# Kernel optimization log

Hardware: AMD Instinct MI355X
Metric: run time of the kernel (lower is better)

Reference implementation:

```python
import jax, jax.numpy as jnp
import numpy as np

N_USERS = 100000
N_ITEMS = 50000
N = N_USERS + N_ITEMS
D = 64
NNZ = 2000000
N_HOPS = 3
EDGE_RATE = 0.5   # note: torch code KEEPS an edge with prob = rate (floor(rate+u))
MESS_RATE = 0.1   # standard dropout: keep prob = 1 - rate


def setup_inputs() -> dict:
    key = jax.random.key(0)
    k1, k2, k3, k4, k5 = jax.random.split(key, 5)
    user_embed = jax.random.normal(k1, (N_USERS, D), dtype=jnp.float32) * 0.1
    item_embed = jax.random.normal(k2, (N_ITEMS, D), dtype=jnp.float32) * 0.1
    edge_rows = jax.random.randint(k3, (NNZ,), 0, N, dtype=jnp.int32)
    edge_cols = jax.random.randint(k4, (NNZ,), 0, N, dtype=jnp.int32)
    edge_vals = jax.random.uniform(k5, (NNZ,), dtype=jnp.float32)
    return {"user_embed": user_embed, "item_embed": item_embed,
            "edge_vals": edge_vals, "edge_rows": edge_rows, "edge_cols": edge_cols}


def reference(user_embed, item_embed, edge_vals, edge_rows, edge_cols):
    # all_embed: [N, D]
    all_embed = jnp.concatenate([user_embed, item_embed], axis=0)
    agg = all_embed
    embs = [all_embed]
    dkey = jax.random.key(42)
    for hop in range(N_HOPS):
        dkey, ke, km = jax.random.split(dkey, 3)
        # sparse edge dropout: torch keeps edge where floor(rate + u) == 1, i.e. u >= 1 - rate
        u = jax.random.uniform(ke, (NNZ,), dtype=jnp.float32)
        keep = (EDGE_RATE + u) >= 1.0
        v = jnp.where(keep, edge_vals, 0.0) * (1.0 / (1.0 - EDGE_RATE))
        # spmm: out[r] += v * agg[c]   -- gather + segment-reduce
        msg = v[:, None] * agg[edge_cols]          # [NNZ, D]
        agg = jax.ops.segment_sum(msg, edge_rows, num_segments=N)  # [N, D]
        # message dropout (standard inverted dropout, p = MESS_RATE)
        mk = jax.random.bernoulli(km, 1.0 - MESS_RATE, agg.shape)
        agg = jnp.where(mk, agg * (1.0 / (1.0 - MESS_RATE)), 0.0)
        embs.append(agg)
    # [N, n_hops+1, D]; user half = out[:N_USERS], item half = out[N_USERS:]
    return jnp.stack(embs, axis=1)
```

## Files before the change

### kernel.cpp

```cpp
#include <hip/hip_runtime.h>
#include <stdint.h>

#define N_USERS 100000
#define N_ITEMS 50000
#define NTOT    150000
#define DIM     64
#define NNZ     2000000
#define NHOPS   3
#define NBLK_SCAN ((NTOT + 255) / 256)
#define NOCT    8
#define OCT_ROWS (NTOT / NOCT)
#define NBUCK   293
#define BCAP    6400
#define HB_ITERS 8

__host__ __device__ inline void tf2x32(uint32_t k0, uint32_t k1,
                                       uint32_t x0, uint32_t x1,
                                       uint32_t& o0, uint32_t& o1) {
  uint32_t ks2 = k0 ^ k1 ^ 0x1BD11BDAu;
  x0 += k0; x1 += k1;
#define ROTL(x,r) (((x) << (r)) | ((x) >> (32 - (r))))
#define RND(r) { x0 += x1; x1 = ROTL(x1, r); x1 ^= x0; }
  RND(13) RND(15) RND(26) RND(6)
  x0 += k1;  x1 += ks2 + 1u;
  RND(17) RND(29) RND(16) RND(24)
  x0 += ks2; x1 += k0 + 2u;
  RND(13) RND(15) RND(26) RND(6)
  x0 += k0;  x1 += k1 + 3u;
  RND(17) RND(29) RND(16) RND(24)
  x0 += k1;  x1 += ks2 + 4u;
  RND(13) RND(15) RND(26) RND(6)
  x0 += ks2; x1 += k0 + 5u;
  o0 = x0; o1 = x1;
#undef RND
#undef ROTL
}

__device__ inline float tf_uniform(uint32_t k0, uint32_t k1, uint32_t idx) {
  uint32_t b1, b2;
  tf2x32(k0, k1, 0u, idx, b1, b2);
  uint32_t bits = b1 ^ b2;
  return __uint_as_float((bits >> 9) | 0x3f800000u) - 1.0f;
}

__device__ inline uint32_t keep_bits(uint32_t e,
                                     uint32_t e00, uint32_t e01,
                                     uint32_t e10, uint32_t e11,
                                     uint32_t e20, uint32_t e21) {
  uint32_t kb = 0u;
  if (0.5f + tf_uniform(e00, e01, e) >= 1.0f) kb |= 1u;
  if (0.5f + tf_uniform(e10, e11, e) >= 1.0f) kb |= 2u;
  if (0.5f + tf_uniform(e20, e21, e) >= 1.0f) kb |= 4u;
  return kb;
}


__global__ __launch_bounds__(256) void k_init(const float4* __restrict__ user,
                                              const float4* __restrict__ item,
                                              float4* __restrict__ out) {
  int idx = blockIdx.x * 256 + threadIdx.x;
  if (idx >= NTOT * 16) return;
  int n = idx >> 4;
  float4 v = (n < N_USERS) ? user[idx] : item[idx - N_USERS * 16];
  out[(size_t)n * 64 + (idx & 15)] = v;
}

__global__ __launch_bounds__(256) void k_hist_bin(const int* __restrict__ rows,
                                                  const int* __restrict__ cols,
                                                  const float* __restrict__ vals,
                                                  uint32_t* __restrict__ cnt,
                                                  uint32_t* __restrict__ gbcur,
                                                  uint2* __restrict__ staging,
                                                  uint32_t e00, uint32_t e01,
                                                  uint32_t e10, uint32_t e11,
                                                  uint32_t e20, uint32_t e21) {
  __shared__ uint32_t bcnt[NBUCK], bbase[NBUCK];
  int t = threadIdx.x;
  int ebase = blockIdx.x * (HB_ITERS * 256);
  for (int b = t; b < NBUCK; b += 256) bcnt[b] = 0u;
  __syncthreads();

  uint32_t srow[HB_ITERS], scol[HB_ITERS], sval[HB_ITERS];
#pragma unroll
  for (int it = 0; it < HB_ITERS; ++it) {
    int e = ebase + it * 256 + t;
    bool valid = (e < NNZ);
    uint32_t kb = valid ? keep_bits((uint32_t)e, e00, e01, e10, e11, e20, e21) : 0u;
    uint32_t row = 0, colkb = 0, v2b = 0;
    if (kb) {
      row = (uint32_t)rows[e];
      colkb = ((uint32_t)cols[e] << 3) | kb;
      v2b = __float_as_uint(vals[e] * 2.0f);
      atomicAdd(&cnt[row], 1u);
      atomicAdd(&bcnt[row >> 9], 1u);
    }
    srow[it] = row; scol[it] = colkb; sval[it] = v2b;
  }
  __syncthreads();
  for (int b = t; b < NBUCK; b += 256) {
    uint32_t c = bcnt[b];
    bbase[b] = c ? atomicAdd(&gbcur[b * 16], c) : 0u;
    bcnt[b] = 0u;
  }
  __syncthreads();
#pragma unroll
  for (int it = 0; it < HB_ITERS; ++it) {
    uint32_t colkb = scol[it];
    if (colkb & 7u) {
      uint32_t row = srow[it];
      uint32_t b = row >> 9;
      uint32_t rank = atomicAdd(&bcnt[b], 1u);
      staging[(size_t)b * BCAP + bbase[b] + rank] =
          make_uint2(((row & 511u) << 21) | colkb, sval[it]);
    }
  }
}

__global__ __launch_bounds__(256) void k_scan1(const uint32_t* __restrict__ cnt,
                                               uint32_t* __restrict__ strt,
                                               uint32_t* __restrict__ part) {
  __shared__ uint32_t s[256];
  int t = threadIdx.x;
  int i = blockIdx.x * 256 + t;
  uint32_t x = (i < NTOT) ? cnt[i] : 0u;
  s[t] = x; __syncthreads();
  for (int off = 1; off < 256; off <<= 1) {
    uint32_t y = (t >= off) ? s[t - off] : 0u;
    __syncthreads();
    s[t] += y;
    __syncthreads();
  }
  if (i < NTOT) strt[i] = s[t] - x;
  if (t == 255) part[blockIdx.x] = s[255];
}

__global__ __launch_bounds__(1024) void k_scan2(uint32_t* __restrict__ part) {
  __shared__ uint32_t s[1024];
  int t = threadIdx.x;
  uint32_t x = (t < NBLK_SCAN) ? part[t] : 0u;
  s[t] = x; __syncthreads();
  for (int off = 1; off < 1024; off <<= 1) {
    uint32_t y = (t >= off) ? s[t - off] : 0u;
    __syncthreads();
    s[t] += y;
    __syncthreads();
  }
  if (t < NBLK_SCAN) part[t] = s[t] - x;
}

__global__ __launch_bounds__(256) void k_scan3(uint32_t* __restrict__ strt,
                                               const uint32_t* __restrict__ part,
                                               uint32_t* __restrict__ cur) {
  int i = blockIdx.x * 256 + threadIdx.x;
  if (i >= NTOT) return;
  uint32_t v = strt[i] + part[i >> 8];
  strt[i] = v;
  cur[i] = v;
}

__global__ __launch_bounds__(1024) void k_sort(const uint2* __restrict__ staging,
                                               const uint32_t* __restrict__ gbcur,
                                               const uint32_t* __restrict__ strt,
                                               uint2* __restrict__ rec) {
  __shared__ uint2 lbuf[BCAP];
  __shared__ uint32_t lcur[512];
  int t = threadIdx.x;
  int b = blockIdx.x;
  int base_row = b << 9;
  uint32_t base_pos = strt[base_row];
  uint32_t n = gbcur[b * 16];
  if (t < 512) {
    int r = base_row + t;
    lcur[t] = (r < NTOT) ? (strt[r] - base_pos) : 0u;
  }
  __syncthreads();
  const uint2* sg = staging + (size_t)b * BCAP;
  for (uint32_t i = t; i < n; i += 1024) {
    uint2 v = sg[i];
    uint32_t rloc = v.x >> 21;
    uint32_t p = atomicAdd(&lcur[rloc], 1u);
    lbuf[p] = make_uint2(v.x & 0x1FFFFFu, v.y);
  }
  __syncthreads();
  for (uint32_t p = t; p < n; p += 1024) {
    rec[base_pos + p] = lbuf[p];
  }
}

__global__ __launch_bounds__(256) void k_hist_fb(const int* __restrict__ rows,
                                                 uint32_t* __restrict__ cnt,
                                                 uint8_t* __restrict__ kbits,
                                                 uint32_t e00, uint32_t e01,
                                                 uint32_t e10, uint32_t e11,
                                                 uint32_t e20, uint32_t e21) {
  int e = blockIdx.x * 256 + threadIdx.x;
  if (e >= NNZ) return;
  uint32_t kb = keep_bits((uint32_t)e, e00, e01, e10, e11, e20, e21);
  int row = rows[e];
  uint32_t oct = (uint32_t)row / OCT_ROWS;
  kbits[e] = (uint8_t)(kb | (oct << 4));
  if (kb) atomicAdd(&cnt[row], 1u);
}

__global__ __launch_bounds__(256) void k_scatter_fb(const float* __restrict__ vals,
                                                    const int* __restrict__ rows,
                                                    const int* __restrict__ cols,
                                                    const uint8_t* __restrict__ kbits,
                                                    uint32_t* __restrict__ cur,
                                                    uint2* __restrict__ rec) {
  int e = (blockIdx.x >> 3) * 256 + threadIdx.x;
  if (e >= NNZ) return;
  uint32_t oct = (uint32_t)(blockIdx.x & 7);
  uint32_t kbv = kbits[e];
  if ((kbv >> 4) != oct) return;
  uint32_t kb = kbv & 7u;
  if (!kb) return;
  uint32_t j = atomicAdd(&cur[rows[e]], 1u);
  rec[j] = make_uint2(((uint32_t)cols[e] << 3) | kb,
                      __float_as_uint(vals[e] * 2.0f));
}

__global__ __launch_bounds__(256) void k_spmm_seg(const uint32_t* __restrict__ strt,
                                                  const uint32_t* __restrict__ cnt,
                                                  const uint2* __restrict__ rec,
                                                  float* __restrict__ out,
                                                  int hop, uint32_t km0, uint32_t km1) {
  int wave = (blockIdx.x * 256 + threadIdx.x) >> 6;
  int lane = threadIdx.x & 63;
  int g = lane >> 4;
  int q = lane & 15;
  int row = wave * 4 + g;
  if (row >= NTOT) return;
  uint32_t s = strt[row];
  uint32_t e = s + cnt[row];
  const uint32_t mask = 1u << hop;
  const float4* srcb = (const float4*)out + (size_t)hop * 16 + q;
  float4 a0 = {0.f,0.f,0.f,0.f}, a1 = a0, a2 = a0, a3 = a0;
  uint32_t j = s;
  for (; j + 4 <= e; j += 4) {
    uint2 r0 = rec[j], r1 = rec[j + 1], r2 = rec[j + 2], r3 = rec[j + 3];
    bool k0 = (r0.x & mask) != 0u, k1 = (r1.x & mask) != 0u;
    bool k2 = (r2.x & mask) != 0u, k3 = (r3.x & mask) != 0u;
    size_t c0 = k0 ? (size_t)(r0.x >> 3) * 64 : 0;
    size_t c1 = k1 ? (size_t)(r1.x >> 3) * 64 : 0;
    size_t c2 = k2 ? (size_t)(r2.x >> 3) * 64 : 0;
    size_t c3 = k3 ? (size_t)(r3.x >> 3) * 64 : 0;
    float4 s0 = srcb[c0], s1 = srcb[c1], s2 = srcb[c2], s3 = srcb[c3];
    float v0 = k0 ? __uint_as_float(r0.y) : 0.f;
    float v1 = k1 ? __uint_as_float(r1.y) : 0.f;
    float v2 = k2 ? __uint_as_float(r2.y) : 0.f;
    float v3 = k3 ? __uint_as_float(r3.y) : 0.f;
    a0.x += v0 * s0.x; a0.y += v0 * s0.y; a0.z += v0 * s0.z; a0.w += v0 * s0.w;
    a1.x += v1 * s1.x; a1.y += v1 * s1.y; a1.z += v1 * s1.z; a1.w += v1 * s1.w;
    a2.x += v2 * s2.x; a2.y += v2 * s2.y; a2.z += v2 * s2.z; a2.w += v2 * s2.w;
    a3.x += v3 * s3.x; a3.y += v3 * s3.y; a3.z += v3 * s3.z; a3.w += v3 * s3.w;
  }
  for (; j < e; ++j) {
    uint2 r = rec[j];
    if (r.x & mask) {
      float v = __uint_as_float(r.y);
      float4 sv = srcb[(size_t)(r.x >> 3) * 64];
      a0.x += v * sv.x; a0.y += v * sv.y; a0.z += v * sv.z; a0.w += v * sv.w;
    }
  }
  float4 acc;
  acc.x = (a0.x + a1.x) + (a2.x + a3.x);
  acc.y = (a0.y + a1.y) + (a2.y + a3.y);
  acc.z = (a0.z + a1.z) + (a2.z + a3.z);
  acc.w = (a0.w + a1.w) + (a2.w + a3.w);
  uint32_t base = (uint32_t)(row * 64 + q * 4);
  float u0 = tf_uniform(km0, km1, base + 0u);
  float u1 = tf_uniform(km0, km1, base + 1u);
  float u2 = tf_uniform(km0, km1, base + 2u);
  float u3 = tf_uniform(km0, km1, base + 3u);
  const float sc = (float)(1.0 / 0.9);
  acc.x = (u0 < 0.9f) ? acc.x * sc : 0.0f;
  acc.y = (u1 < 0.9f) ? acc.y * sc : 0.0f;
  acc.z = (u2 < 0.9f) ? acc.z * sc : 0.0f;
  acc.w = (u3 < 0.9f) ? acc.w * sc : 0.0f;
  ((float4*)(out + ((size_t)row * 4 + hop + 1) * 64))[q] = acc;
}

extern "C" void kernel_launch(void* const* d_in, const int* in_sizes, int n_in,
                              void* d_out, int out_size, void* d_ws, size_t ws_size,
                              hipStream_t stream) {
  const float* user = (const float*)d_in[0];
  const float* item = (const float*)d_in[1];
  const float* vals = (const float*)d_in[2];
  const int*   rows = (const int*)d_in[3];
  const int*   cols = (const int*)d_in[4];
  float* out = (float*)d_out;

  char* w = (char*)d_ws;
  uint32_t* cnt     = (uint32_t*)(w);
  uint32_t* gbcur   = (uint32_t*)(w + 600000);
  uint32_t* strt    = (uint32_t*)(w + 618752);
  uint32_t* cur     = (uint32_t*)(w + 1218752);
  uint32_t* part    = (uint32_t*)(w + 1818752);
  uint2*    rec     = (uint2*)   (w + 1822848);
  uint2*    staging = (uint2*)   (w + 17822848);
  uint8_t*  kbits   = (uint8_t*) (w + 17822848);
  const size_t NEEDED = 17822848 + (size_t)NBUCK * BCAP * 8;
  bool big = ws_size >= NEEDED;

  uint32_t k0 = 0u, k1 = 42u;
  uint32_t ke[NHOPS][2], km[NHOPS][2];
  for (int h = 0; h < NHOPS; ++h) {
    uint32_t nk0, nk1;
    tf2x32(k0, k1, 0u, 0u, nk0, nk1);
    tf2x32(k0, k1, 0u, 1u, ke[h][0], ke[h][1]);
    tf2x32(k0, k1, 0u, 2u, km[h][0], km[h][1]);
    k0 = nk0; k1 = nk1;
  }

  hipMemsetAsync(cnt, 0, 618752, stream);
  if (big) {
    k_hist_bin<<<(NNZ + HB_ITERS * 256 - 1) / (HB_ITERS * 256), 256, 0, stream>>>(
        rows, cols, vals, cnt, gbcur, staging,
        ke[0][0], ke[0][1], ke[1][0], ke[1][1], ke[2][0], ke[2][1]);
  } else {
    k_hist_fb<<<(NNZ + 255) / 256, 256, 0, stream>>>(
        rows, cnt, kbits,
        ke[0][0], ke[0][1], ke[1][0], ke[1][1], ke[2][0], ke[2][1]);
  }
  k_scan1<<<NBLK_SCAN, 256, 0, stream>>>(cnt, strt, part);
  k_scan2<<<1, 1024, 0, stream>>>(part);
  k_scan3<<<NBLK_SCAN, 256, 0, stream>>>(strt, part, cur);
  if (big) {
    k_sort<<<NBUCK, 1024, 0, stream>>>(staging, gbcur, strt, rec);
  } else {
    k_scatter_fb<<<NOCT * ((NNZ + 255) / 256), 256, 0, stream>>>(
        vals, rows, cols, kbits, cur, rec);
  }
  k_init<<<(NTOT * 16 + 255) / 256, 256, 0, stream>>>(
      (const float4*)user, (const float4*)item, (float4*)out);

  for (int h = 0; h < NHOPS; ++h) {
    k_spmm_seg<<<((NTOT + 3) / 4 * 64 + 255) / 256, 256, 0, stream>>>(
        strt, cnt, rec, out, h, km[h][0], km[h][1]);
  }
}
```

Baseline: 289.3 us.

## Derive per-row CSR offsets inside bucket sort, dropping global row histogram and scans

The binning kernel no longer does global per-row atomic counts. It only counts per 512-row bucket and keeps the keep-bits in shared memory, re-reading rows, cols and vals in its second pass instead of holding them in registers. A single-block scan over bucket totals replaces the three-kernel row scan, and each sort block builds its own per-row counts, runs a local prefix sum and writes strt and cnt. This removes the global atomics and two launches, but the binning kernel now loads the edge arrays twice and the sort block uses twice as much shared memory, which may lower occupancy.

```diff
diff --git a/kernel.cpp b/kernel.cpp
--- a/kernel.cpp
+++ b/kernel.cpp
@@ -12,7 +12,7 @@
 #define OCT_ROWS (NTOT / NOCT)
 #define NBUCK   293
 #define BCAP    6400
-#define HB_ITERS 8
+#define HB_EDGES 4096
 
 __host__ __device__ inline void tf2x32(uint32_t k0, uint32_t k1,
                                        uint32_t x0, uint32_t x1,
@@ -68,33 +68,22 @@
 __global__ __launch_bounds__(256) void k_hist_bin(const int* __restrict__ rows,
                                                   const int* __restrict__ cols,
                                                   const float* __restrict__ vals,
-                                                  uint32_t* __restrict__ cnt,
                                                   uint32_t* __restrict__ gbcur,
                                                   uint2* __restrict__ staging,
                                                   uint32_t e00, uint32_t e01,
                                                   uint32_t e10, uint32_t e11,
                                                   uint32_t e20, uint32_t e21) {
   __shared__ uint32_t bcnt[NBUCK], bbase[NBUCK];
-  int t = threadIdx.x;
-  int ebase = blockIdx.x * (HB_ITERS * 256);
+  __shared__ uint8_t lkb[HB_EDGES];
+  int t = threadIdx.x;
+  int ebase = blockIdx.x * HB_EDGES;
   for (int b = t; b < NBUCK; b += 256) bcnt[b] = 0u;
   __syncthreads();
-
-  uint32_t srow[HB_ITERS], scol[HB_ITERS], sval[HB_ITERS];
-#pragma unroll
-  for (int it = 0; it < HB_ITERS; ++it) {
+  for (int it = 0; it < HB_EDGES / 256; ++it) {
     int e = ebase + it * 256 + t;
-    bool valid = (e < NNZ);
-    uint32_t kb = valid ? keep_bits((uint32_t)e, e00, e01, e10, e11, e20, e21) : 0u;
-    uint32_t row = 0, colkb = 0, v2b = 0;
-    if (kb) {
-      row = (uint32_t)rows[e];
-      colkb = ((uint32_t)cols[e] << 3) | kb;
-      v2b = __float_as_uint(vals[e] * 2.0f);
-      atomicAdd(&cnt[row], 1u);
-      atomicAdd(&bcnt[row >> 9], 1u);
-    }
-    srow[it] = row; scol[it] = colkb; sval[it] = v2b;
+    uint32_t kb = (e < NNZ) ? keep_bits((uint32_t)e, e00, e01, e10, e11, e20, e21) : 0u;
+    lkb[it * 256 + t] = (uint8_t)kb;
+    if (kb) atomicAdd(&bcnt[(uint32_t)rows[e] >> 9], 1u);
   }
   __syncthreads();
   for (int b = t; b < NBUCK; b += 256) {
@@ -103,88 +92,79 @@
     bcnt[b] = 0u;
   }
   __syncthreads();
-#pragma unroll
-  for (int it = 0; it < HB_ITERS; ++it) {
-    uint32_t colkb = scol[it];
-    if (colkb & 7u) {
-      uint32_t row = srow[it];
+  for (int it = 0; it < HB_EDGES / 256; ++it) {
+    int e = ebase + it * 256 + t;
+    uint32_t kb = (e < NNZ) ? (uint32_t)lkb[it * 256 + t] : 0u;
+    if (kb) {
+      uint32_t row = (uint32_t)rows[e];
       uint32_t b = row >> 9;
       uint32_t rank = atomicAdd(&bcnt[b], 1u);
       staging[(size_t)b * BCAP + bbase[b] + rank] =
-          make_uint2(((row & 511u) << 21) | colkb, sval[it]);
+          make_uint2(((row & 511u) << 21) | ((uint32_t)cols[e] << 3) | kb,
+                     __float_as_uint(vals[e] * 2.0f));
     }
   }
 }
 
-__global__ __launch_bounds__(256) void k_scan1(const uint32_t* __restrict__ cnt,
-                                               uint32_t* __restrict__ strt,
-                                               uint32_t* __restrict__ part) {
-  __shared__ uint32_t s[256];
-  int t = threadIdx.x;
-  int i = blockIdx.x * 256 + t;
-  uint32_t x = (i < NTOT) ? cnt[i] : 0u;
+__global__ __launch_bounds__(512) void k_bscan(const uint32_t* __restrict__ gbcur,
+                                               uint32_t* __restrict__ bstart) {
+  __shared__ uint32_t s[512];
+  int t = threadIdx.x;
+  uint32_t x = (t < NBUCK) ? gbcur[t * 16] : 0u;
   s[t] = x; __syncthreads();
-  for (int off = 1; off < 256; off <<= 1) {
+  for (int off = 1; off < 512; off <<= 1) {
     uint32_t y = (t >= off) ? s[t - off] : 0u;
     __syncthreads();
     s[t] += y;
     __syncthreads();
   }
-  if (i < NTOT) strt[i] = s[t] - x;
-  if (t == 255) part[blockIdx.x] = s[255];
-}
-
-__global__ __launch_bounds__(1024) void k_scan2(uint32_t* __restrict__ part) {
-  __shared__ uint32_t s[1024];
-  int t = threadIdx.x;
-  uint32_t x = (t < NBLK_SCAN) ? part[t] : 0u;
-  s[t] = x; __syncthreads();
-  for (int off = 1; off < 1024; off <<= 1) {
-    uint32_t y = (t >= off) ? s[t - off] : 0u;
-    __syncthreads();
-    s[t] += y;
-    __syncthreads();
-  }
-  if (t < NBLK_SCAN) part[t] = s[t] - x;
-}
-
-__global__ __launch_bounds__(256) void k_scan3(uint32_t* __restrict__ strt,
-                                               const uint32_t* __restrict__ part,
-                                               uint32_t* __restrict__ cur) {
-  int i = blockIdx.x * 256 + threadIdx.x;
-  if (i >= NTOT) return;
-  uint32_t v = strt[i] + part[i >> 8];
-  strt[i] = v;
-  cur[i] = v;
+  if (t < NBUCK) bstart[t] = s[t] - x;
 }
 
 __global__ __launch_bounds__(1024) void k_sort(const uint2* __restrict__ staging,
                                                const uint32_t* __restrict__ gbcur,
-                                               const uint32_t* __restrict__ strt,
-                                               uint2* __restrict__ rec) {
-  __shared__ uint2 lbuf[BCAP];
-  __shared__ uint32_t lcur[512];
+                                               const uint32_t* __restrict__ bstart,
+                                               uint2* __restrict__ rec,
+                                               uint32_t* __restrict__ strt,
+                                               uint32_t* __restrict__ cnt) {
+  __shared__ uint2 lraw[BCAP];
+  __shared__ uint2 lout[BCAP];
+  __shared__ uint32_t lcnt[512], lcur[512];
   int t = threadIdx.x;
   int b = blockIdx.x;
   int base_row = b << 9;
-  uint32_t base_pos = strt[base_row];
   uint32_t n = gbcur[b * 16];
-  if (t < 512) {
-    int r = base_row + t;
-    lcur[t] = (r < NTOT) ? (strt[r] - base_pos) : 0u;
-  }
+  uint32_t base_pos = bstart[b];
+  if (t < 512) lcnt[t] = 0u;
   __syncthreads();
   const uint2* sg = staging + (size_t)b * BCAP;
   for (uint32_t i = t; i < n; i += 1024) {
     uint2 v = sg[i];
-    uint32_t rloc = v.x >> 21;
-    uint32_t p = atomicAdd(&lcur[rloc], 1u);
-    lbuf[p] = make_uint2(v.x & 0x1FFFFFu, v.y);
-  }
-  __syncthreads();
-  for (uint32_t p = t; p < n; p += 1024) {
-    rec[base_pos + p] = lbuf[p];
-  }
+    lraw[i] = v;
+    atomicAdd(&lcnt[v.x >> 21], 1u);
+  }
+  __syncthreads();
+  uint32_t myc = (t < 512) ? lcnt[t] : 0u;
+  for (int off = 1; off < 512; off <<= 1) {
+    uint32_t y = (t < 512 && t >= off) ? lcnt[t - off] : 0u;
+    __syncthreads();
+    if (t < 512) lcnt[t] += y;
+    __syncthreads();
+  }
+  if (t < 512) {
+    uint32_t excl = lcnt[t] - myc;
+    lcur[t] = excl;
+    int r = base_row + t;
+    if (r < NTOT) { strt[r] = base_pos + excl; cnt[r] = myc; }
+  }
+  __syncthreads();
+  for (uint32_t i = t; i < n; i += 1024) {
+    uint2 v = lraw[i];
+    uint32_t p = atomicAdd(&lcur[v.x >> 21], 1u);
+    lout[p] = make_uint2(v.x & 0x1FFFFFu, v.y);
+  }
+  __syncthreads();
+  for (uint32_t i = t; i < n; i += 1024) rec[base_pos + i] = lout[i];
 }
 
 __global__ __launch_bounds__(256) void k_hist_fb(const int* __restrict__ rows,
@@ -200,6 +180,48 @@
   uint32_t oct = (uint32_t)row / OCT_ROWS;
   kbits[e] = (uint8_t)(kb | (oct << 4));
   if (kb) atomicAdd(&cnt[row], 1u);
+}
+
+__global__ __launch_bounds__(256) void k_scan1(const uint32_t* __restrict__ cnt,
+                                               uint32_t* __restrict__ strt,
+                                               uint32_t* __restrict__ part) {
+  __shared__ uint32_t s[256];
+  int t = threadIdx.x;
+  int i = blockIdx.x * 256 + t;
+  uint32_t x = (i < NTOT) ? cnt[i] : 0u;
+  s[t] = x; __syncthreads();
+  for (int off = 1; off < 256; off <<= 1) {
+    uint32_t y = (t >= off) ? s[t - off] : 0u;
+    __syncthreads();
+    s[t] += y;
+    __syncthreads();
+  }
+  if (i < NTOT) strt[i] = s[t] - x;
+  if (t == 255) part[blockIdx.x] = s[255];
+}
+
+__global__ __launch_bounds__(1024) void k_scan2(uint32_t* __restrict__ part) {
+  __shared__ uint32_t s[1024];
+  int t = threadIdx.x;
+  uint32_t x = (t < NBLK_SCAN) ? part[t] : 0u;
+  s[t] = x; __syncthreads();
+  for (int off = 1; off < 1024; off <<= 1) {
+    uint32_t y = (t >= off) ? s[t - off] : 0u;
+    __syncthreads();
+    s[t] += y;
+    __syncthreads();
+  }
+  if (t < NBLK_SCAN) part[t] = s[t] - x;
+}
+
+__global__ __launch_bounds__(256) void k_scan3(uint32_t* __restrict__ strt,
+                                               const uint32_t* __restrict__ part,
+                                               uint32_t* __restrict__ cur) {
+  int i = blockIdx.x * 256 + threadIdx.x;
+  if (i >= NTOT) return;
+  uint32_t v = strt[i] + part[i >> 8];
+  strt[i] = v;
+  cur[i] = v;
 }
 
 __global__ __launch_bounds__(256) void k_scatter_fb(const float* __restrict__ vals,
@@ -292,15 +314,16 @@
   float* out = (float*)d_out;
 
   char* w = (char*)d_ws;
-  uint32_t* cnt     = (uint32_t*)(w);
-  uint32_t* gbcur   = (uint32_t*)(w + 600000);
-  uint32_t* strt    = (uint32_t*)(w + 618752);
-  uint32_t* cur     = (uint32_t*)(w + 1218752);
-  uint32_t* part    = (uint32_t*)(w + 1818752);
-  uint2*    rec     = (uint2*)   (w + 1822848);
-  uint2*    staging = (uint2*)   (w + 17822848);
-  uint8_t*  kbits   = (uint8_t*) (w + 17822848);
-  const size_t NEEDED = 17822848 + (size_t)NBUCK * BCAP * 8;
+  uint32_t* gbcur   = (uint32_t*)(w);
+  uint32_t* bstart  = (uint32_t*)(w + 18752);
+  uint32_t* strt    = (uint32_t*)(w + 22848);
+  uint32_t* cnt     = (uint32_t*)(w + 622848);
+  uint32_t* cur     = (uint32_t*)(w + 1222848);
+  uint32_t* part    = (uint32_t*)(w + 1822848);
+  uint2*    rec     = (uint2*)   (w + 1826944);
+  uint2*    staging = (uint2*)   (w + 17826944);
+  uint8_t*  kbits   = (uint8_t*) (w + 17826944);
+  const size_t NEEDED = 17826944 + (size_t)NBUCK * BCAP * 8;
   bool big = ws_size >= NEEDED;
 
   uint32_t k0 = 0u, k1 = 42u;
@@ -313,22 +336,21 @@
     k0 = nk0; k1 = nk1;
   }
 
-  hipMemsetAsync(cnt, 0, 618752, stream);
   if (big) {
-    k_hist_bin<<<(NNZ + HB_ITERS * 256 - 1) / (HB_ITERS * 256), 256, 0, stream>>>(
-        rows, cols, vals, cnt, gbcur, staging,
+    hipMemsetAsync(gbcur, 0, 18752, stream);
+    k_hist_bin<<<(NNZ + HB_EDGES - 1) / HB_EDGES, 256, 0, stream>>>(
+        rows, cols, vals, gbcur, staging,
         ke[0][0], ke[0][1], ke[1][0], ke[1][1], ke[2][0], ke[2][1]);
+    k_bscan<<<1, 512, 0, stream>>>(gbcur, bstart);
+    k_sort<<<NBUCK, 1024, 0, stream>>>(staging, gbcur, bstart, rec, strt, cnt);
   } else {
+    hipMemsetAsync(cnt, 0, 600000, stream);
     k_hist_fb<<<(NNZ + 255) / 256, 256, 0, stream>>>(
         rows, cnt, kbits,
         ke[0][0], ke[0][1], ke[1][0], ke[1][1], ke[2][0], ke[2][1]);
-  }
-  k_scan1<<<NBLK_SCAN, 256, 0, stream>>>(cnt, strt, part);
-  k_scan2<<<1, 1024, 0, stream>>>(part);
-  k_scan3<<<NBLK_SCAN, 256, 0, stream>>>(strt, part, cur);
-  if (big) {
-    k_sort<<<NBUCK, 1024, 0, stream>>>(staging, gbcur, strt, rec);
-  } else {
+    k_scan1<<<NBLK_SCAN, 256, 0, stream>>>(cnt, strt, part);
+    k_scan2<<<1, 1024, 0, stream>>>(part);
+    k_scan3<<<NBLK_SCAN, 256, 0, stream>>>(strt, part, cur);
     k_scatter_fb<<<NOCT * ((NNZ + 255) / 256), 256, 0, stream>>>(
         vals, rows, cols, kbits, cur, rec);
   }
```

Result: faster. 239.2 us, median of 2 (-17.3%).
